# Kernel optimization log

Measured on AMD Instinct MI355X. Metric: run time of the kernel, lower is better.

Reference implementation:

```python
import jax, jax.numpy as jnp
import numpy as np

N_POINTS = 12288
FEAT_DIM = 16


def setup_inputs() -> dict:
    key = jax.random.key(0)
    feats = jax.random.normal(key, (N_POINTS, FEAT_DIM), dtype=jnp.float32)
    return {"feats": feats, "topK": 1}


def reference(feats, topK):
    """LOGG3D_ATTN eval path for a single point cloud (batch=1).

    feats: [N, D] post-spvcnn point features.
    1) self_attention -> scalar weight per point
    2) weight features, top-k select k = N*topK points
    3) SOP: mean second-order (outer-product) pooling, flatten, L2-normalize.
    """
    N, D = feats.shape
    inv_sqrt_d = 1.0 / jnp.sqrt(jnp.asarray(D, feats.dtype))
    # self-attention over points: [N, N] scores (the ridge-regime hot spot)
    scores = jnp.matmul(feats, feats.T) * inv_sqrt_d          # [N, N]
    attn = jax.nn.softmax(scores, axis=-1)                    # [N, N]
    ctx = jnp.matmul(attn, feats)                             # [N, D]
    weights = jax.nn.sigmoid(jnp.sum(ctx * feats, axis=-1, keepdims=True))  # [N, 1]

    weighted_feat = feats * weights                           # [N, D]
    k = int(N * topK)
    _, top_idx = jax.lax.top_k(weights[:, 0], k)              # [k]
    x = weighted_feat[top_idx][None, :, :]                    # [1, k, D]

    # SOP: mean outer-product pooling (signed_sqrt=False, do_fc=False)
    so = jnp.einsum('bnd,bne->bde', x, x) / k                 # [1, D, D]
    out = so.reshape(1, -1)                                   # [1, D*D]
    out = out / jnp.linalg.norm(out, axis=-1, keepdims=True)
    return out
```

## Files before the change

### kernel.cpp

```cpp
#include <hip/hip_runtime.h>
#include <hip/hip_bf16.h>
#include <math.h>


#define NP 12288
#define JSPLIT 32
#define JCHUNK (NP / JSPLIT)
#define JT JCHUNK
#define JGPT (JT / 16)

#define QSCALE 0.3606737602222839f

typedef __attribute__((ext_vector_type(4))) float f32x4;
typedef __attribute__((ext_vector_type(2))) unsigned u32x2;
typedef __attribute__((ext_vector_type(8))) short s16x8;
typedef __attribute__((ext_vector_type(4))) short s16x4;

#if defined(__has_builtin)
#if __has_builtin(__builtin_amdgcn_mfma_f32_16x16x16bf16_1k)
#define HAVE_MFMA16_BUILTIN 1
#endif
#if __has_builtin(__builtin_amdgcn_exp2f)
#define EXP2F(x) __builtin_amdgcn_exp2f(x)
#endif
#if __has_builtin(__builtin_amdgcn_perm)
#define HAVE_PERM 1
#endif
#endif
#ifndef EXP2F
#define EXP2F(x) exp2f(x)
#endif

static __device__ __forceinline__ f32x4 mfma16(s16x4 a, s16x4 b, f32x4 c) {
#ifdef HAVE_MFMA16_BUILTIN
    return __builtin_amdgcn_mfma_f32_16x16x16bf16_1k(a, b, c, 0, 0, 0);
#else
    f32x4 d;
    asm volatile("s_nop 1\n\t"
                 "v_mfma_f32_16x16x16_bf16 %0, %1, %2, %0"
                 : "=v"(d)
                 : "v"(a), "v"(b), "0"(c));
    return d;
#endif
}

static __device__ __forceinline__ short f2bf(float x) {
    __hip_bfloat16 h = __float2bfloat16(x);
    return __builtin_bit_cast(short, h);
}

static __device__ __forceinline__ s16x4 pack_rhu(f32x4 e) {
    const unsigned u0 = __builtin_bit_cast(unsigned, e[0]) + 0x8000u;
    const unsigned u1 = __builtin_bit_cast(unsigned, e[1]) + 0x8000u;
    const unsigned u2 = __builtin_bit_cast(unsigned, e[2]) + 0x8000u;
    const unsigned u3 = __builtin_bit_cast(unsigned, e[3]) + 0x8000u;
    u32x2 t;
#ifdef HAVE_PERM
    t[0] = __builtin_amdgcn_perm(u1, u0, 0x07060302u);
    t[1] = __builtin_amdgcn_perm(u3, u2, 0x07060302u);
#else
    t[0] = (u0 >> 16) | (u1 & 0xFFFF0000u);
    t[1] = (u2 >> 16) | (u3 & 0xFFFF0000u);
#endif
    return __builtin_bit_cast(s16x4, t);
}

static __device__ __forceinline__ f32x4 exp4(f32x4 s) {
    f32x4 e;
    e[0] = EXP2F(s[0]); e[1] = EXP2F(s[1]);
    e[2] = EXP2F(s[2]); e[3] = EXP2F(s[3]);
    return e;
}

__global__ __launch_bounds__(256)
void prep(const float* __restrict__ feats,
          unsigned short* __restrict__ ghi, unsigned short* __restrict__ shi,
          unsigned short* __restrict__ gFt)
{
    __shared__ unsigned short tr[64 * 16];
    const int tid = threadIdx.x;
    const int rowbase = blockIdx.x * 64;

    const f32x4 v = *(const f32x4*)(feats + (size_t)rowbase * 16 + tid * 4);
    s16x4 hv, sv;
    #pragma unroll
    for (int k = 0; k < 4; ++k) {
        hv[k] = f2bf(v[k]);
        sv[k] = f2bf(v[k] * QSCALE);
    }
    *(s16x4*)(ghi + (size_t)rowbase * 16 + tid * 4) = hv;
    *(s16x4*)(shi + (size_t)rowbase * 16 + tid * 4) = sv;
    *(s16x4*)(tr + (tid >> 2) * 16 + (tid & 3) * 4) = hv;
    __syncthreads();

    if (tid < 128) {
        const int p = tid >> 3, q8 = tid & 7;
        s16x8 o;
        #pragma unroll
        for (int e = 0; e < 8; ++e) o[e] = (short)tr[(q8 * 8 + e) * 16 + p];
        *(s16x8*)(gFt + (size_t)p * NP + rowbase + q8 * 8) = o;
    }
}

__global__ __launch_bounds__(256)
void attn_mfma(const unsigned short* __restrict__ ghi,
               const unsigned short* __restrict__ shi,
               const unsigned short* __restrict__ gFt,
               float* __restrict__ ctx_part,
               float* __restrict__ l_part)
{
    __shared__ unsigned short hiT[JT * 16];
    __shared__ unsigned short FtT[16 * JT];

    const int tid = threadIdx.x;
    const int wave = tid >> 6, lane = tid & 63;
    const int il = lane & 15, g = lane >> 4, g4 = g * 4, g8 = g * 8;
    const int js = blockIdx.x & (JSPLIT - 1);
    const int rowblk = blockIdx.x >> 5;
    const int ibase = rowblk * 256 + wave * 64;
    const int jbase = js * JCHUNK;

    s16x4 bF[4];
    #pragma unroll
    for (int t = 0; t < 4; ++t)
        bF[t] = *(const s16x4*)(shi + (size_t)(ibase + t * 16 + il) * 16 + g4);

    s16x4 ones; ones[0] = ones[1] = ones[2] = ones[3] = (short)0x3F80;
    const f32x4 kZero = {0.f, 0.f, 0.f, 0.f};
    f32x4 ctx[4], lacc[4];
    #pragma unroll
    for (int t = 0; t < 4; ++t) { ctx[t] = kZero; lacc[t] = kZero; }

    const char* aBase = (const char*)hiT + ((il * 32 + g8) ^ ((il & 7) << 4));
    const char* vPlane = (const char*)FtT + il * (JT * 2);
    const int vKey = (il & 7) << 4;

    const int fp = tid >> 4, fq = tid & 15;

    {
        const char* gH = (const char*)ghi + (size_t)jbase * 32;
        #pragma unroll
        for (int k = 0; k < 3; ++k) {
            const int c = tid + (k << 8);
            s16x8 v = *(const s16x8*)(gH + c * 16);
            *(s16x8*)((char*)hiT + ((c * 16) ^ (((c >> 1) & 7) << 4))) = v;
        }
        const char* gF = (const char*)gFt + (size_t)fp * (NP * 2) + (size_t)jbase * 2;
        #pragma unroll
        for (int k = 0; k < 3; ++k) {
            const int cq = fq + (k << 4);
            s16x8 v = *(const s16x8*)(gF + cq * 16);
            *(s16x8*)((char*)FtT + fp * (JT * 2)
                      + ((cq * 16) ^ ((fp & 7) << 4))) = v;
        }
    }
    __syncthreads();

    #pragma unroll 2
    for (int jg = 0; jg < JGPT; ++jg) {
        const s16x4 aS = *(const s16x4*)(aBase + jg * 512);
        const s16x4 aV = *(const s16x4*)(vPlane + (((jg << 5) + g8) ^ vKey));
        #pragma unroll
        for (int t = 0; t < 4; ++t) {
            const f32x4 s = mfma16(aS, bF[t], kZero);
            const s16x4 p = pack_rhu(exp4(s));
            ctx[t]  = mfma16(aV, p, ctx[t]);
            lacc[t] = mfma16(ones, p, lacc[t]);
        }
    }

    asm volatile("s_nop 7\n\ts_nop 7" ::: );

    #pragma unroll
    for (int t = 0; t < 4; ++t) {
        const int iT = ibase + t * 16 + il;
        *(f32x4*)(ctx_part + ((size_t)js * NP + iT) * 16 + g4) = ctx[t];
        if (g == 0) l_part[(size_t)js * NP + iT] = lacc[t][0];
    }
}

__global__ __launch_bounds__(256)
void weights_sop(const float* __restrict__ feats,
                 const float* __restrict__ ctxp,
                 const float* __restrict__ lp,
                 float* __restrict__ mpart)
{
    __shared__ float gw[64 * 16];
    const int tid = threadIdx.x;
    const int rl = tid >> 2, q = tid & 3, d0 = q * 4;
    const int row = blockIdx.x * 64 + rl;

    f32x4 c = {0.f, 0.f, 0.f, 0.f};
    float l = 0.f;
    #pragma unroll 8
    for (int js = 0; js < JSPLIT; ++js) {
        c += *(const f32x4*)(ctxp + ((size_t)js * NP + row) * 16 + d0);
        l += lp[(size_t)js * NP + row];
    }
    const f32x4 fv = *(const f32x4*)(feats + (size_t)row * 16 + d0);
    float zp = c[0]*fv[0] + c[1]*fv[1] + c[2]*fv[2] + c[3]*fv[3];
    zp += __shfl_xor(zp, 1, 64);
    zp += __shfl_xor(zp, 2, 64);
    const float z = zp / l;
    const float w = 1.f / (1.f + EXP2F(-z * 1.4426950408889634f));

    f32x4 gv; gv[0] = w*fv[0]; gv[1] = w*fv[1]; gv[2] = w*fv[2]; gv[3] = w*fv[3];
    *(f32x4*)(gw + rl * 16 + d0) = gv;
    __syncthreads();

    const int d = tid >> 4, e = tid & 15;
    float acc = 0.f;
    #pragma unroll 8
    for (int r = 0; r < 64; ++r)
        acc += gw[r * 16 + d] * gw[r * 16 + e];
    mpart[(size_t)blockIdx.x * 256 + tid] = acc;
}

__global__ __launch_bounds__(1024)
void finalize(const float* __restrict__ mpart, float* __restrict__ out)
{
    __shared__ float part[1024];
    __shared__ float red[4];
    const int tid = threadIdx.x;
    const int o = tid & 255, s = tid >> 8;

    float m = 0.f;
    #pragma unroll 4
    for (int b = s; b < 192; b += 4) m += mpart[(size_t)b * 256 + o];
    part[tid] = m;
    __syncthreads();

    if (tid < 256) {
        m = part[tid] + part[tid + 256] + part[tid + 512] + part[tid + 768];
        float ss = m * m;
        #pragma unroll
        for (int msk = 32; msk >= 1; msk >>= 1) ss += __shfl_xor(ss, msk, 64);
        if ((tid & 63) == 0) red[tid >> 6] = ss;
    }
    __syncthreads();
    if (tid < 256) {
        const float tot = red[0] + red[1] + red[2] + red[3];
        out[tid] = m / sqrtf(tot);
    }
}

extern "C" void kernel_launch(void* const* d_in, const int* in_sizes, int n_in,
                              void* d_out, int out_size, void* d_ws, size_t ws_size,
                              hipStream_t stream) {
    (void)n_in; (void)out_size; (void)ws_size;
    const float* feats = (const float*)d_in[0];

    char* w = (char*)d_ws;
    unsigned short* ghi = (unsigned short*)(w);
    unsigned short* shi = (unsigned short*)(w + 393216);
    unsigned short* gFt = (unsigned short*)(w + 786432);
    float* ctxp = (float*)(w + 1179648);
    float* lp   = (float*)(w + 26345472);
    float* mp   = (float*)(w + 27918336);

    prep       <<<192,  256, 0, stream>>>(feats, ghi, shi, gFt);
    attn_mfma  <<<1536, 256, 0, stream>>>(ghi, shi, gFt, ctxp, lp);
    weights_sop<<<192,  256, 0, stream>>>(feats, ctxp, lp, mp);
    finalize   <<<1,    1024, 0, stream>>>(mp, (float*)d_out);
}
```

Baseline: 94.57 us.

## Halve attention j-split and shrink weights/SOP blocks to 64 threads

Reduces the column split of the attention kernel from 32 to 16 chunks, doubling per-block work and LDS tile size while halving the partial ctx/l buffers written and re-read. The weights/SOP kernel becomes 768 single-wave blocks of 16 rows each, with a padded shared tile and four outputs per thread, and finalize reduces over 768 partials. The goal is less partial-sum traffic and more parallelism in the reduction stage, at the cost of fewer attention blocks (768 on a large GPU) and more partial SOP matrices to sum.

```diff
diff --git a/kernel.cpp b/kernel.cpp
--- a/kernel.cpp
+++ b/kernel.cpp
@@ -4,10 +4,11 @@
 
 
 #define NP 12288
-#define JSPLIT 32
+#define JSPLIT 16
 #define JCHUNK (NP / JSPLIT)
 #define JT JCHUNK
 #define JGPT (JT / 16)
+#define NBLK2 768
 
 #define QSCALE 0.3606737602222839f
 
@@ -116,7 +117,7 @@
     const int wave = tid >> 6, lane = tid & 63;
     const int il = lane & 15, g = lane >> 4, g4 = g * 4, g8 = g * 8;
     const int js = blockIdx.x & (JSPLIT - 1);
-    const int rowblk = blockIdx.x >> 5;
+    const int rowblk = blockIdx.x >> 4;
     const int ibase = rowblk * 256 + wave * 64;
     const int jbase = js * JCHUNK;
 
@@ -140,14 +141,14 @@
     {
         const char* gH = (const char*)ghi + (size_t)jbase * 32;
         #pragma unroll
-        for (int k = 0; k < 3; ++k) {
+        for (int k = 0; k < 6; ++k) {
             const int c = tid + (k << 8);
             s16x8 v = *(const s16x8*)(gH + c * 16);
             *(s16x8*)((char*)hiT + ((c * 16) ^ (((c >> 1) & 7) << 4))) = v;
         }
         const char* gF = (const char*)gFt + (size_t)fp * (NP * 2) + (size_t)jbase * 2;
         #pragma unroll
-        for (int k = 0; k < 3; ++k) {
+        for (int k = 0; k < 6; ++k) {
             const int cq = fq + (k << 4);
             s16x8 v = *(const s16x8*)(gF + cq * 16);
             *(s16x8*)((char*)FtT + fp * (JT * 2)
@@ -179,20 +180,20 @@
     }
 }
 
-__global__ __launch_bounds__(256)
-void weights_sop(const float* __restrict__ feats,
-                 const float* __restrict__ ctxp,
-                 const float* __restrict__ lp,
-                 float* __restrict__ mpart)
-{
-    __shared__ float gw[64 * 16];
+__global__ __launch_bounds__(64)
+void wsop(const float* __restrict__ feats,
+          const float* __restrict__ ctxp,
+          const float* __restrict__ lp,
+          float* __restrict__ mpart)
+{
+    __shared__ float gw[16][17];
     const int tid = threadIdx.x;
     const int rl = tid >> 2, q = tid & 3, d0 = q * 4;
-    const int row = blockIdx.x * 64 + rl;
+    const int row = blockIdx.x * 16 + rl;
 
     f32x4 c = {0.f, 0.f, 0.f, 0.f};
     float l = 0.f;
-    #pragma unroll 8
+    #pragma unroll
     for (int js = 0; js < JSPLIT; ++js) {
         c += *(const f32x4*)(ctxp + ((size_t)js * NP + row) * 16 + d0);
         l += lp[(size_t)js * NP + row];
@@ -204,16 +205,21 @@
     const float z = zp / l;
     const float w = 1.f / (1.f + EXP2F(-z * 1.4426950408889634f));
 
-    f32x4 gv; gv[0] = w*fv[0]; gv[1] = w*fv[1]; gv[2] = w*fv[2]; gv[3] = w*fv[3];
-    *(f32x4*)(gw + rl * 16 + d0) = gv;
-    __syncthreads();
-
-    const int d = tid >> 4, e = tid & 15;
-    float acc = 0.f;
-    #pragma unroll 8
-    for (int r = 0; r < 64; ++r)
-        acc += gw[r * 16 + d] * gw[r * 16 + e];
-    mpart[(size_t)blockIdx.x * 256 + tid] = acc;
+    gw[rl][d0 + 0] = w * fv[0];
+    gw[rl][d0 + 1] = w * fv[1];
+    gw[rl][d0 + 2] = w * fv[2];
+    gw[rl][d0 + 3] = w * fv[3];
+    __syncthreads();
+
+    #pragma unroll
+    for (int k = 0; k < 4; ++k) {
+        const int idx = tid * 4 + k;
+        const int dd = idx >> 4, ee = idx & 15;
+        float acc = 0.f;
+        #pragma unroll
+        for (int r = 0; r < 16; ++r) acc += gw[r][dd] * gw[r][ee];
+        mpart[(size_t)blockIdx.x * 256 + idx] = acc;
+    }
 }
 
 __global__ __launch_bounds__(1024)
@@ -225,8 +231,8 @@
     const int o = tid & 255, s = tid >> 8;
 
     float m = 0.f;
-    #pragma unroll 4
-    for (int b = s; b < 192; b += 4) m += mpart[(size_t)b * 256 + o];
+    #pragma unroll 8
+    for (int b = s; b < NBLK2; b += 4) m += mpart[(size_t)b * 256 + o];
     part[tid] = m;
     __syncthreads();
 
@@ -255,11 +261,11 @@
     unsigned short* shi = (unsigned short*)(w + 393216);
     unsigned short* gFt = (unsigned short*)(w + 786432);
     float* ctxp = (float*)(w + 1179648);
-    float* lp   = (float*)(w + 26345472);
-    float* mp   = (float*)(w + 27918336);
-
-    prep       <<<192,  256, 0, stream>>>(feats, ghi, shi, gFt);
-    attn_mfma  <<<1536, 256, 0, stream>>>(ghi, shi, gFt, ctxp, lp);
-    weights_sop<<<192,  256, 0, stream>>>(feats, ctxp, lp, mp);
-    finalize   <<<1,    1024, 0, stream>>>(mp, (float*)d_out);
-}
+    float* lp   = (float*)(w + 13762560);
+    float* mp   = (float*)(w + 14548992);
+
+    prep     <<<192,   256, 0, stream>>>(feats, ghi, shi, gFt);
+    attn_mfma<<<768,   256, 0, stream>>>(ghi, shi, gFt, ctxp, lp);
+    wsop     <<<NBLK2,  64, 0, stream>>>(feats, ctxp, lp, mp);
+    finalize <<<1,    1024, 0, stream>>>(mp, (float*)d_out);
+}
```

Measured after the change: 96.65 us. +2.2%, slower.
